# Optimization experiments

Hardware: AMD Instinct MI355X
Metric: run time of the kernel (lower is better)

The kernel has to match this reference:

```python
import jax, jax.numpy as jnp
import numpy as np


def setup_inputs() -> dict:
    key = jax.random.key(0)
    k1, k2, k3, k4 = jax.random.split(key, 4)
    B, S, H, E, I = 2, 2048, 1024, 8, 2048
    return {
        "x": jax.random.normal(k1, (B, S, H), jnp.float32),
        "Wg": jax.random.normal(k2, (H, E), jnp.float32) * 0.02,      # router weight
        "W_in": jax.random.normal(k3, (E, H, 2 * I), jnp.float32) * 0.02,  # gated FFN in
        "W_out": jax.random.normal(k4, (E, I, H), jnp.float32) * 0.02,      # FFN out
        "top_k": 2,
    }


def reference(x, Wg, W_in, W_out, top_k):
    B, S, H = x.shape
    E = Wg.shape[1]
    xt = x.reshape(B * S, H)                      # [T, H]
    T = xt.shape[0]

    # Router: logits -> top-k -> softmax over selected experts -> dense gates
    logits = xt @ Wg                              # [T, E]
    tk_logits, tk_idx = jax.lax.top_k(logits, top_k)
    tk_gates = jax.nn.softmax(tk_logits, axis=1).astype(x.dtype)
    dense_gates = jnp.zeros((T, E), x.dtype).at[jnp.arange(T)[:, None], tk_idx].set(tk_gates)

    # All-experts MLP (calibrate_all_experts path: same math as sparse routing)
    h = jnp.einsum('th,ehd->etd', xt, W_in)       # [E, T, 2I]
    g, u = jnp.split(h, 2, axis=-1)               # gated FFN chunks
    a = jax.nn.silu(g) * u                        # [E, T, I]
    y = jnp.einsum('eti,eih->eth', a, W_out)      # [E, T, H]

    out = jnp.einsum('eth,te->th', y, dense_gates)  # combine with gates
    return out.reshape(B, S, H)
```

## Files before the change

### kernel.cpp

```cpp
#include <hip/hip_runtime.h>
#include <hip/hip_bf16.h>

#define T_TOKENS 4096
#define H_DIM    1024
#define E_EXP    8
#define I_DIM    2048

typedef short bf16x8 __attribute__((ext_vector_type(8)));
typedef float f32x4  __attribute__((ext_vector_type(4)));

#define SWZ(r) (((r) >> 1) & 3)

__device__ inline unsigned short f2bf(float f) {
  union { __hip_bfloat16 h; unsigned short u; } c;
  c.h = __float2bfloat16(f);
  return c.u;
}
__device__ inline float bf2f(unsigned short u) {
  union { unsigned int i; float f; } c;
  c.i = (unsigned int)u << 16;
  return c.f;
}

__device__ inline void load16_lds(const void* g, void* l) {
  __builtin_amdgcn_global_load_lds(
      (const __attribute__((address_space(1))) unsigned int*)g,
      (__attribute__((address_space(3))) unsigned int*)l, 16, 0, 0);
}

__global__ void cast_bf16_kernel(const float* __restrict__ in,
                                 unsigned short* __restrict__ out, int n) {
  int i = (blockIdx.x * blockDim.x + threadIdx.x) * 4;
  if (i >= n) return;
  float4 v = *(const float4*)(in + i);
  ushort4 o;
  o.x = f2bf(v.x); o.y = f2bf(v.y); o.z = f2bf(v.z); o.w = f2bf(v.w);
  *(ushort4*)(out + i) = o;
}

__global__ void cast_transpose_kernel(const float* __restrict__ in,
                                      unsigned short* __restrict__ out,
                                      int K, int N) {
  __shared__ float tile[64][33];
  const float* src = in + (size_t)blockIdx.z * K * N;
  unsigned short* dst = out + (size_t)blockIdx.z * K * N;
  int n0 = blockIdx.x * 32, k0 = blockIdx.y * 64;
  int tid = threadIdx.x;
#pragma unroll
  for (int r = 0; r < 8; r++) {
    int idx = r * 256 + tid;
    int kk = idx >> 5, nn = idx & 31;
    tile[kk][nn] = src[(size_t)(k0 + kk) * N + n0 + nn];
  }
  __syncthreads();
  int n = tid >> 3, kg = tid & 7;
  __align__(16) unsigned short o[8];
#pragma unroll
  for (int j = 0; j < 8; j++) o[j] = f2bf(tile[kg * 8 + j][n]);
  *(uint4*)&dst[(size_t)(n0 + n) * K + k0 + kg * 8] = *(uint4*)o;
}

__global__ void router_kernel(const float* __restrict__ x, const float* __restrict__ Wg,
                              int* __restrict__ counts, int* __restrict__ list_tok,
                              float* __restrict__ list_gate, int* __restrict__ tok_codes) {
  int t = blockIdx.x;
  int lane = threadIdx.x;
  float acc[8];
#pragma unroll
  for (int e = 0; e < 8; e++) acc[e] = 0.f;
  const float* xr = x + (size_t)t * H_DIM;
  for (int h = lane; h < H_DIM; h += 64) {
    float xv = xr[h];
    const float4* w = (const float4*)(Wg + (size_t)h * 8);
    float4 w0 = w[0], w1 = w[1];
    acc[0] += xv * w0.x; acc[1] += xv * w0.y; acc[2] += xv * w0.z; acc[3] += xv * w0.w;
    acc[4] += xv * w1.x; acc[5] += xv * w1.y; acc[6] += xv * w1.z; acc[7] += xv * w1.w;
  }
#pragma unroll
  for (int off = 32; off > 0; off >>= 1)
#pragma unroll
    for (int e = 0; e < 8; e++) acc[e] += __shfl_xor(acc[e], off, 64);
  if (lane == 0) {
    int e1 = 0; float l1 = acc[0];
    for (int e = 1; e < 8; e++) if (acc[e] > l1) { l1 = acc[e]; e1 = e; }
    int e2 = -1; float l2 = -1e30f;
    for (int e = 0; e < 8; e++) if (e != e1 && acc[e] > l2) { l2 = acc[e]; e2 = e; }
    float g1 = 1.f / (1.f + expf(l2 - l1));
    float g2 = 1.f - g1;
    int p1 = atomicAdd(&counts[e1], 1);
    list_tok[e1 * T_TOKENS + p1] = t; list_gate[e1 * T_TOKENS + p1] = g1;
    int p2 = atomicAdd(&counts[e2], 1);
    list_tok[e2 * T_TOKENS + p2] = t; list_gate[e2 * T_TOKENS + p2] = g2;
    tok_codes[2 * t]     = e1 * T_TOKENS + p1;
    tok_codes[2 * t + 1] = e2 * T_TOKENS + p2;
  }
}

__global__ void prefix_kernel(const int* __restrict__ counts, int* __restrict__ base) {
  if (threadIdx.x == 0) {
    int s = 0;
    for (int e = 0; e < 8; e++) { base[e] = s; s += counts[e]; }
  }
}

__global__ __launch_bounds__(256) void gemm1_kernel(
    const unsigned short* __restrict__ xb,
    const unsigned short* __restrict__ w_in_t,
    const int* __restrict__ counts, const int* __restrict__ base,
    const int* __restrict__ list_tok,
    unsigned short* __restrict__ a_buf)
{
  int e = blockIdx.z;
  int Ne = counts[e];
  int row0 = blockIdx.y * 128;
  if (row0 >= Ne) return;
  int ib = blockIdx.x * 64;
  const unsigned short* W = w_in_t + (size_t)e * 4096 * 1024;
  int slot_base = base[e];

  __shared__ __align__(16) unsigned short As[128 * 32];
  __shared__ __align__(16) unsigned short Bs[128 * 32];
  __shared__ int toks[128];

  int tid = threadIdx.x;
  if (tid < 128) {
    int pos = row0 + tid;
    toks[tid] = list_tok[e * T_TOKENS + (pos < Ne ? pos : 0)];
  }
  __syncthreads();

  int wv = tid >> 6, lane = tid & 63;

  const unsigned short* srcA[2];
  const unsigned short* srcB[2];
  unsigned short* ldsA[2];
  unsigned short* ldsB[2];
#pragma unroll
  for (int d = 0; d < 2; d++) {
    int r = 32 * wv + 16 * d + (lane >> 2);
    int kg = (lane & 3) ^ SWZ(r);
    srcA[d] = xb + (size_t)toks[r] * H_DIM + kg * 8;
    int c = r >> 6, q = (r >> 4) & 3, rr = r & 15;
    int wrow = (q & 1) * 2048 + ib + 32 * c + (q >> 1) * 16 + rr;
    srcB[d] = W + (size_t)wrow * H_DIM + kg * 8;
    ldsA[d] = As + (32 * wv + 16 * d) * 32;
    ldsB[d] = Bs + (32 * wv + 16 * d) * 32;
  }

  int rh = wv >> 1, ch = wv & 1;
  int l15 = lane & 15, quad = lane >> 4;

  f32x4 acc[4][4] = {};

  for (int k0 = 0; k0 < H_DIM; k0 += 32) {
    load16_lds(srcA[0] + k0, ldsA[0]);
    load16_lds(srcA[1] + k0, ldsA[1]);
    load16_lds(srcB[0] + k0, ldsB[0]);
    load16_lds(srcB[1] + k0, ldsB[1]);
    __syncthreads();

    bf16x8 af[4], bf[4];
#pragma unroll
    for (int rb = 0; rb < 4; rb++) {
      int row = rh * 64 + rb * 16 + l15;
      int kg = quad ^ SWZ(row);
      af[rb] = *(const bf16x8*)&As[row * 32 + kg * 8];
    }
#pragma unroll
    for (int cb = 0; cb < 4; cb++) {
      int brow = ch * 64 + cb * 16 + l15;
      int kg = quad ^ SWZ(brow);
      bf[cb] = *(const bf16x8*)&Bs[brow * 32 + kg * 8];
    }
#pragma unroll
    for (int rb = 0; rb < 4; rb++)
#pragma unroll
      for (int cb = 0; cb < 4; cb++)
        acc[rb][cb] = __builtin_amdgcn_mfma_f32_16x16x32_bf16(af[rb], bf[cb], acc[rb][cb], 0, 0, 0);
    __syncthreads();
  }

#pragma unroll
  for (int rb = 0; rb < 4; rb++)
#pragma unroll
    for (int cp = 0; cp < 2; cp++) {
      int icol = ib + 32 * ch + cp * 16 + l15;
#pragma unroll
      for (int v = 0; v < 4; v++) {
        int row = rh * 64 + rb * 16 + quad * 4 + v;
        int pos = row0 + row;
        if (pos < Ne) {
          float g = acc[rb][2 * cp][v], u = acc[rb][2 * cp + 1][v];
          float a = g / (1.f + __expf(-g)) * u;
          a_buf[(size_t)(slot_base + pos) * I_DIM + icol] = f2bf(a);
        }
      }
    }
}

__global__ __launch_bounds__(256) void gemm2_kernel(
    const unsigned short* __restrict__ a_buf,
    const unsigned short* __restrict__ w_out_t,
    const int* __restrict__ counts, const int* __restrict__ base,
    const float* __restrict__ list_gate,
    unsigned short* __restrict__ y_buf)
{
  int e = blockIdx.z;
  int Ne = counts[e];
  int row0 = blockIdx.y * 128;
  if (row0 >= Ne) return;
  int hb = blockIdx.x * 128;
  const unsigned short* W = w_out_t + (size_t)e * 1024 * 2048;
  int slot_base = base[e];

  __shared__ __align__(16) unsigned short As[128 * 32];
  __shared__ __align__(16) unsigned short Bs[128 * 32];
  __shared__ float gts[128];

  int tid = threadIdx.x;
  if (tid < 128) {
    int pos = row0 + tid;
    gts[tid] = list_gate[e * T_TOKENS + (pos < Ne ? pos : Ne - 1)];
  }

  int wv = tid >> 6, lane = tid & 63;
  const unsigned short* srcA[2];
  const unsigned short* srcB[2];
  unsigned short* ldsA[2];
  unsigned short* ldsB[2];
#pragma unroll
  for (int d = 0; d < 2; d++) {
    int r = 32 * wv + 16 * d + (lane >> 2);
    int kg = (lane & 3) ^ SWZ(r);
    int pos = row0 + r;
    int slot = slot_base + (pos < Ne ? pos : Ne - 1);
    srcA[d] = a_buf + (size_t)slot * I_DIM + kg * 8;
    srcB[d] = W + (size_t)(hb + r) * I_DIM + kg * 8;
    ldsA[d] = As + (32 * wv + 16 * d) * 32;
    ldsB[d] = Bs + (32 * wv + 16 * d) * 32;
  }

  int rh = wv >> 1, ch = wv & 1;
  int l15 = lane & 15, quad = lane >> 4;

  f32x4 acc[4][4] = {};

  for (int k0 = 0; k0 < I_DIM; k0 += 32) {
    load16_lds(srcA[0] + k0, ldsA[0]);
    load16_lds(srcA[1] + k0, ldsA[1]);
    load16_lds(srcB[0] + k0, ldsB[0]);
    load16_lds(srcB[1] + k0, ldsB[1]);
    __syncthreads();

    bf16x8 af[4], bf[4];
#pragma unroll
    for (int rb = 0; rb < 4; rb++) {
      int row = rh * 64 + rb * 16 + l15;
      int kg = quad ^ SWZ(row);
      af[rb] = *(const bf16x8*)&As[row * 32 + kg * 8];
    }
#pragma unroll
    for (int cb = 0; cb < 4; cb++) {
      int brow = ch * 64 + cb * 16 + l15;
      int kg = quad ^ SWZ(brow);
      bf[cb] = *(const bf16x8*)&Bs[brow * 32 + kg * 8];
    }
#pragma unroll
    for (int rb = 0; rb < 4; rb++)
#pragma unroll
      for (int cb = 0; cb < 4; cb++)
        acc[rb][cb] = __builtin_amdgcn_mfma_f32_16x16x32_bf16(af[rb], bf[cb], acc[rb][cb], 0, 0, 0);
    __syncthreads();
  }

#pragma unroll
  for (int rb = 0; rb < 4; rb++)
#pragma unroll
    for (int cb = 0; cb < 4; cb++) {
      int col = hb + ch * 64 + cb * 16 + l15;
#pragma unroll
      for (int v = 0; v < 4; v++) {
        int row = rh * 64 + rb * 16 + quad * 4 + v;
        int pos = row0 + row;
        if (pos < Ne)
          y_buf[(size_t)(slot_base + pos) * H_DIM + col] = f2bf(gts[row] * acc[rb][cb][v]);
      }
    }
}

__global__ void combine_kernel(const unsigned short* __restrict__ y_buf,
                               const int* __restrict__ tok_codes,
                               const int* __restrict__ base,
                               float* __restrict__ out) {
  int t = blockIdx.x;
  int c0 = tok_codes[2 * t], c1 = tok_codes[2 * t + 1];
  int s0 = base[c0 / T_TOKENS] + (c0 % T_TOKENS);
  int s1 = base[c1 / T_TOKENS] + (c1 % T_TOKENS);
  int h = threadIdx.x * 4;
  ushort4 a = *(const ushort4*)&y_buf[(size_t)s0 * H_DIM + h];
  ushort4 b = *(const ushort4*)&y_buf[(size_t)s1 * H_DIM + h];
  float4 o;
  o.x = bf2f(a.x) + bf2f(b.x);
  o.y = bf2f(a.y) + bf2f(b.y);
  o.z = bf2f(a.z) + bf2f(b.z);
  o.w = bf2f(a.w) + bf2f(b.w);
  *(float4*)&out[(size_t)t * H_DIM + h] = o;
}

extern "C" void kernel_launch(void* const* d_in, const int* in_sizes, int n_in,
                              void* d_out, int out_size, void* d_ws, size_t ws_size,
                              hipStream_t stream) {
  const float* x     = (const float*)d_in[0];
  const float* Wg    = (const float*)d_in[1];
  const float* W_in  = (const float*)d_in[2];
  const float* W_out = (const float*)d_in[3];

  char* ws = (char*)d_ws;
  size_t off = 0;
  auto alloc = [&](size_t bytes) {
    char* p = ws + off;
    off += (bytes + 255) & ~(size_t)255;
    return p;
  };
  unsigned short* xb      = (unsigned short*)alloc((size_t)T_TOKENS * H_DIM * 2);
  unsigned short* w_in_t  = (unsigned short*)alloc((size_t)E_EXP * 2 * I_DIM * H_DIM * 2);
  unsigned short* w_out_t = (unsigned short*)alloc((size_t)E_EXP * H_DIM * I_DIM * 2);
  unsigned short* a_buf   = (unsigned short*)alloc((size_t)2 * T_TOKENS * I_DIM * 2);
  int*   counts    = (int*)alloc(E_EXP * 4);
  int*   base      = (int*)alloc(E_EXP * 4);
  int*   list_tok  = (int*)alloc((size_t)E_EXP * T_TOKENS * 4);
  float* list_gate = (float*)alloc((size_t)E_EXP * T_TOKENS * 4);
  int*   tok_codes = (int*)alloc((size_t)2 * T_TOKENS * 4);
  if (off > ws_size) return;

  unsigned short* y_buf = w_in_t;

  hipMemsetAsync(counts, 0, E_EXP * 4, stream);

  cast_bf16_kernel<<<(T_TOKENS * H_DIM / 4 + 255) / 256, 256, 0, stream>>>(x, xb, T_TOKENS * H_DIM);
  cast_transpose_kernel<<<dim3(4096 / 32, 1024 / 64, E_EXP), 256, 0, stream>>>(W_in, w_in_t, 1024, 4096);
  cast_transpose_kernel<<<dim3(1024 / 32, 2048 / 64, E_EXP), 256, 0, stream>>>(W_out, w_out_t, 2048, 1024);
  router_kernel<<<T_TOKENS, 64, 0, stream>>>(x, Wg, counts, list_tok, list_gate, tok_codes);
  prefix_kernel<<<1, 1, 0, stream>>>(counts, base);
  gemm1_kernel<<<dim3(I_DIM / 64, T_TOKENS / 128, E_EXP), 256, 0, stream>>>(
      xb, w_in_t, counts, base, list_tok, a_buf);
  gemm2_kernel<<<dim3(H_DIM / 128, T_TOKENS / 128, E_EXP), 256, 0, stream>>>(
      a_buf, w_out_t, counts, base, list_gate, y_buf);
  combine_kernel<<<T_TOKENS, 256, 0, stream>>>(y_buf, tok_codes, base, (float*)d_out);
}
```

Measured before the change: 540.8 us.

## Fuse weight cast-transposes, x cast and router into one prep kernel

Merges the x bf16 cast, both weight cast-transpose kernels and the router into a single launch, with the x cast folded into the router's read of x. Transpose tiles grow to 64x64 and are loaded as float4. Expert slot assignment moves from per-token global atomics to a single-block schedule kernel using shared-memory atomics, and that kernel also computes the prefix base, which removes the memset and the prefix launch. The goal is fewer launches and fewer passes over memory. The serial one-block schedule and the reordered token lists within each expert are the trade-offs.

```diff
diff --git a/kernel.cpp b/kernel.cpp
--- a/kernel.cpp
+++ b/kernel.cpp
@@ -28,49 +28,41 @@
       (__attribute__((address_space(3))) unsigned int*)l, 16, 0, 0);
 }
 
-__global__ void cast_bf16_kernel(const float* __restrict__ in,
-                                 unsigned short* __restrict__ out, int n) {
-  int i = (blockIdx.x * blockDim.x + threadIdx.x) * 4;
-  if (i >= n) return;
-  float4 v = *(const float4*)(in + i);
-  ushort4 o;
-  o.x = f2bf(v.x); o.y = f2bf(v.y); o.z = f2bf(v.z); o.w = f2bf(v.w);
-  *(ushort4*)(out + i) = o;
-}
-
-__global__ void cast_transpose_kernel(const float* __restrict__ in,
-                                      unsigned short* __restrict__ out,
-                                      int K, int N) {
-  __shared__ float tile[64][33];
-  const float* src = in + (size_t)blockIdx.z * K * N;
-  unsigned short* dst = out + (size_t)blockIdx.z * K * N;
-  int n0 = blockIdx.x * 32, k0 = blockIdx.y * 64;
-  int tid = threadIdx.x;
-#pragma unroll
-  for (int r = 0; r < 8; r++) {
-    int idx = r * 256 + tid;
-    int kk = idx >> 5, nn = idx & 31;
-    tile[kk][nn] = src[(size_t)(k0 + kk) * N + n0 + nn];
+__device__ inline void do_transpose(const float* __restrict__ src,
+                                    unsigned short* __restrict__ dst,
+                                    int K, int N, int kb, int nb,
+                                    float (*tile)[65], int tid) {
+  int k0 = kb * 64, n0 = nb * 64;
+#pragma unroll
+  for (int i = 0; i < 4; i++) {
+    int row = (tid >> 4) + i * 16;
+    int col4 = (tid & 15) * 4;
+    float4 v = *(const float4*)(src + (size_t)(k0 + row) * N + n0 + col4);
+    tile[row][col4] = v.x; tile[row][col4 + 1] = v.y;
+    tile[row][col4 + 2] = v.z; tile[row][col4 + 3] = v.w;
   }
   __syncthreads();
-  int n = tid >> 3, kg = tid & 7;
-  __align__(16) unsigned short o[8];
-#pragma unroll
-  for (int j = 0; j < 8; j++) o[j] = f2bf(tile[kg * 8 + j][n]);
-  *(uint4*)&dst[(size_t)(n0 + n) * K + k0 + kg * 8] = *(uint4*)o;
-}
-
-__global__ void router_kernel(const float* __restrict__ x, const float* __restrict__ Wg,
-                              int* __restrict__ counts, int* __restrict__ list_tok,
-                              float* __restrict__ list_gate, int* __restrict__ tok_codes) {
-  int t = blockIdx.x;
-  int lane = threadIdx.x;
+#pragma unroll
+  for (int s = 0; s < 2; s++) {
+    int n = s * 32 + (tid >> 3), kg = tid & 7;
+    __align__(16) unsigned short o[8];
+#pragma unroll
+    for (int j = 0; j < 8; j++) o[j] = f2bf(tile[kg * 8 + j][n]);
+    *(uint4*)&dst[(size_t)(n0 + n) * K + k0 + kg * 8] = *(uint4*)o;
+  }
+}
+
+__device__ inline void do_router(const float* __restrict__ x, const float* __restrict__ Wg,
+                                 unsigned short* __restrict__ xb, int t, int lane,
+                                 int2* __restrict__ te, float2* __restrict__ tg) {
   float acc[8];
 #pragma unroll
   for (int e = 0; e < 8; e++) acc[e] = 0.f;
   const float* xr = x + (size_t)t * H_DIM;
+  unsigned short* xbr = xb + (size_t)t * H_DIM;
   for (int h = lane; h < H_DIM; h += 64) {
     float xv = xr[h];
+    xbr[h] = f2bf(xv);
     const float4* w = (const float4*)(Wg + (size_t)h * 8);
     float4 w0 = w[0], w1 = w[1];
     acc[0] += xv * w0.x; acc[1] += xv * w0.y; acc[2] += xv * w0.z; acc[3] += xv * w0.w;
@@ -86,20 +78,55 @@
     int e2 = -1; float l2 = -1e30f;
     for (int e = 0; e < 8; e++) if (e != e1 && acc[e] > l2) { l2 = acc[e]; e2 = e; }
     float g1 = 1.f / (1.f + expf(l2 - l1));
-    float g2 = 1.f - g1;
-    int p1 = atomicAdd(&counts[e1], 1);
-    list_tok[e1 * T_TOKENS + p1] = t; list_gate[e1 * T_TOKENS + p1] = g1;
-    int p2 = atomicAdd(&counts[e2], 1);
-    list_tok[e2 * T_TOKENS + p2] = t; list_gate[e2 * T_TOKENS + p2] = g2;
-    tok_codes[2 * t]     = e1 * T_TOKENS + p1;
-    tok_codes[2 * t + 1] = e2 * T_TOKENS + p2;
-  }
-}
-
-__global__ void prefix_kernel(const int* __restrict__ counts, int* __restrict__ base) {
-  if (threadIdx.x == 0) {
+    te[t] = make_int2(e1, e2);
+    tg[t] = make_float2(g1, 1.f - g1);
+  }
+}
+
+__global__ __launch_bounds__(256) void prep_kernel(
+    const float* __restrict__ W_in, const float* __restrict__ W_out,
+    const float* __restrict__ x, const float* __restrict__ Wg,
+    unsigned short* __restrict__ w_in_t, unsigned short* __restrict__ w_out_t,
+    unsigned short* __restrict__ xb, int2* __restrict__ te, float2* __restrict__ tg) {
+  __shared__ float tile[64][65];
+  int id = blockIdx.x, tid = threadIdx.x;
+  if (id < 8192) {
+    int e = id >> 10, r = id & 1023, nb = r & 63, kb = r >> 6;
+    do_transpose(W_in + (size_t)e * 1024 * 4096, w_in_t + (size_t)e * 4096 * 1024,
+                 1024, 4096, kb, nb, tile, tid);
+  } else if (id < 12288) {
+    int t2 = id - 8192;
+    int e = t2 >> 9, r = t2 & 511, nb = r & 15, kb = r >> 4;
+    do_transpose(W_out + (size_t)e * 2048 * 1024, w_out_t + (size_t)e * 1024 * 2048,
+                 2048, 1024, kb, nb, tile, tid);
+  } else {
+    int t = (id - 12288) * 4 + (tid >> 6);
+    do_router(x, Wg, xb, t, tid & 63, te, tg);
+  }
+}
+
+__global__ __launch_bounds__(256) void schedule_kernel(
+    const int2* __restrict__ te, const float2* __restrict__ tg,
+    int* __restrict__ counts, int* __restrict__ base,
+    int* __restrict__ list_tok, float* __restrict__ list_gate,
+    int* __restrict__ tok_codes) {
+  __shared__ int cnt[8];
+  int tid = threadIdx.x;
+  if (tid < 8) cnt[tid] = 0;
+  __syncthreads();
+  for (int t = tid; t < T_TOKENS; t += 256) {
+    int2 e = te[t]; float2 g = tg[t];
+    int p1 = atomicAdd(&cnt[e.x], 1);
+    list_tok[e.x * T_TOKENS + p1] = t; list_gate[e.x * T_TOKENS + p1] = g.x;
+    tok_codes[2 * t] = e.x * T_TOKENS + p1;
+    int p2 = atomicAdd(&cnt[e.y], 1);
+    list_tok[e.y * T_TOKENS + p2] = t; list_gate[e.y * T_TOKENS + p2] = g.y;
+    tok_codes[2 * t + 1] = e.y * T_TOKENS + p2;
+  }
+  __syncthreads();
+  if (tid == 0) {
     int s = 0;
-    for (int e = 0; e < 8; e++) { base[e] = s; s += counts[e]; }
+    for (int e = 0; e < 8; e++) { base[e] = s; counts[e] = cnt[e]; s += cnt[e]; }
   }
 }
 
@@ -331,17 +358,14 @@
   int*   list_tok  = (int*)alloc((size_t)E_EXP * T_TOKENS * 4);
   float* list_gate = (float*)alloc((size_t)E_EXP * T_TOKENS * 4);
   int*   tok_codes = (int*)alloc((size_t)2 * T_TOKENS * 4);
+  int2*  te        = (int2*)alloc((size_t)T_TOKENS * 8);
+  float2* tg       = (float2*)alloc((size_t)T_TOKENS * 8);
   if (off > ws_size) return;
 
   unsigned short* y_buf = w_in_t;
 
-  hipMemsetAsync(counts, 0, E_EXP * 4, stream);
-
-  cast_bf16_kernel<<<(T_TOKENS * H_DIM / 4 + 255) / 256, 256, 0, stream>>>(x, xb, T_TOKENS * H_DIM);
-  cast_transpose_kernel<<<dim3(4096 / 32, 1024 / 64, E_EXP), 256, 0, stream>>>(W_in, w_in_t, 1024, 4096);
-  cast_transpose_kernel<<<dim3(1024 / 32, 2048 / 64, E_EXP), 256, 0, stream>>>(W_out, w_out_t, 2048, 1024);
-  router_kernel<<<T_TOKENS, 64, 0, stream>>>(x, Wg, counts, list_tok, list_gate, tok_codes);
-  prefix_kernel<<<1, 1, 0, stream>>>(counts, base);
+  prep_kernel<<<13312, 256, 0, stream>>>(W_in, W_out, x, Wg, w_in_t, w_out_t, xb, te, tg);
+  schedule_kernel<<<1, 256, 0, stream>>>(te, tg, counts, base, list_tok, list_gate, tok_codes);
   gemm1_kernel<<<dim3(I_DIM / 64, T_TOKENS / 128, E_EXP), 256, 0, stream>>>(
       xb, w_in_t, counts, base, list_tok, a_buf);
   gemm2_kernel<<<dim3(H_DIM / 128, T_TOKENS / 128, E_EXP), 256, 0, stream>>>(
```

After: 443.5 us. 1.22x faster.
